# Kernel tuning notes

Hardware: AMD Instinct MI355X
Metric: run time of the kernel (lower is better)

## Reference

```python
import jax, jax.numpy as jnp
import numpy as np

N_NODES = 100000
N_EDGES = 800000
D_DATA = 100
H_DIM = 256
N_CLS = 47
K = 10
ALPHA = 0.1


def setup_inputs() -> dict:
    key = jax.random.key(0)
    ks = jax.random.split(key, 7)
    x = jax.random.normal(ks[0], (N_NODES, D_DATA), dtype=jnp.float32)
    src = jax.random.randint(ks[1], (N_EDGES,), 0, N_NODES, dtype=jnp.int32)
    dst = jax.random.randint(ks[2], (N_EDGES,), 0, N_NODES, dtype=jnp.int32)
    W1 = jax.random.normal(ks[3], (D_DATA, H_DIM), dtype=jnp.float32) / np.sqrt(D_DATA)
    b1 = jax.random.normal(ks[4], (H_DIM,), dtype=jnp.float32) * 0.01
    W2 = jax.random.normal(ks[5], (H_DIM, N_CLS), dtype=jnp.float32) / np.sqrt(H_DIM)
    b2 = jax.random.normal(ks[6], (N_CLS,), dtype=jnp.float32) * 0.01
    return {"x": x, "src": src, "dst": dst, "W1": W1, "b1": b1, "W2": W2, "b2": b2}


def reference(x, src, dst, W1, b1, W2, b2):
    # --- APPNPConv: K steps of symmetric-normalized SpMM + teleport ---
    # DGL normalizes with in-degree^{-1/2} on both message source and output.
    deg = jax.ops.segment_sum(jnp.ones((N_EDGES,), x.dtype), dst, num_segments=N_NODES)
    norm = jax.lax.rsqrt(jnp.maximum(deg, 1.0))[:, None]  # [N,1]
    h = x
    for _ in range(K):
        msg = (h * norm)[src]                              # gather src feats, [E,D]
        agg = jax.ops.segment_sum(msg, dst, num_segments=N_NODES)
        h = (1.0 - ALPHA) * (agg * norm) + ALPHA * x
    # --- feat_trans MLP (dropout inactive in eval) ---
    z = jax.nn.relu(h @ W1 + b1)
    logits = z @ W2 + b2
    return logits
```

## Files before the change

kernel.cpp:

```cpp
#include <hip/hip_runtime.h>
#include <hip/hip_fp16.h>


#define N_NODES 100000
#define N_PAD   100032
#define N_EDGES 800000
#define D_DATA  100
#define H_DIM   256
#define N_CLS   47
#define K_STEPS 10
#define ALPHA   0.1f
#define HS      128
#define MB      64

#define SCAN_NB    200
#define SCAN_CHUNK 500
#define EW_CAP (N_EDGES + 3 * N_NODES)

typedef _Float16 half8_t __attribute__((ext_vector_type(8)));
typedef float floatx4 __attribute__((ext_vector_type(4)));


__global__ void deg_kernel(const int* __restrict__ dst, int* __restrict__ deg, int e) {
    int i = blockIdx.x * blockDim.x + threadIdx.x;
    if (i < e) atomicAdd(&deg[dst[i]], 1);
}

__global__ __launch_bounds__(256) void scan_partial_kernel(
        const int* __restrict__ deg, int* __restrict__ partials) {
    __shared__ int red[256];
    int t = threadIdx.x;
    int base = blockIdx.x * SCAN_CHUNK;
    int s = 0;
    int i0 = 2 * t, i1 = 2 * t + 1;
    if (i0 < SCAN_CHUNK) s += (deg[base + i0] + 3) & ~3;
    if (i1 < SCAN_CHUNK) s += (deg[base + i1] + 3) & ~3;
    red[t] = s;
    __syncthreads();
    for (int off = 128; off > 0; off >>= 1) {
        if (t < off) red[t] += red[t + off];
        __syncthreads();
    }
    if (t == 0) partials[blockIdx.x] = red[0];
}

__global__ __launch_bounds__(256) void scan_top_kernel(
        const int* __restrict__ partials, int* __restrict__ pofs,
        int* __restrict__ row_ptr) {
    __shared__ int s[256];
    int t = threadIdx.x;
    s[t] = (t < SCAN_NB) ? partials[t] : 0;
    __syncthreads();
    for (int off = 1; off < 256; off <<= 1) {
        int v = (t >= off) ? s[t - off] : 0;
        __syncthreads();
        s[t] += v;
        __syncthreads();
    }
    if (t < SCAN_NB) pofs[t] = s[t] - partials[t];
    if (t == SCAN_NB - 1) row_ptr[N_NODES] = s[t];
}

__global__ __launch_bounds__(256) void scan_emit_kernel(
        const int* __restrict__ deg, const int* __restrict__ pofs,
        int* __restrict__ row_ptr, float* __restrict__ norm) {
    __shared__ int s[256];
    int t = threadIdx.x;
    int base = blockIdx.x * SCAN_CHUNK;
    int i0 = 2 * t, i1 = 2 * t + 1;
    int d0 = (i0 < SCAN_CHUNK) ? deg[base + i0] : 0;
    int d1 = (i1 < SCAN_CHUNK) ? deg[base + i1] : 0;
    int p0 = (d0 + 3) & ~3, p1 = (d1 + 3) & ~3;
    s[t] = p0 + p1;
    __syncthreads();
    for (int off = 1; off < 256; off <<= 1) {
        int v = (t >= off) ? s[t - off] : 0;
        __syncthreads();
        s[t] += v;
        __syncthreads();
    }
    int p = s[t] - (p0 + p1) + pofs[blockIdx.x];
    if (i0 < SCAN_CHUNK) {
        row_ptr[base + i0] = p;
        norm[base + i0] = rsqrtf((float)max(d0, 1));
    }
    if (i1 < SCAN_CHUNK) {
        row_ptr[base + i1] = p + p0;
        norm[base + i1] = rsqrtf((float)max(d1, 1));
    }
}

__global__ void scatter_kernel(const int* __restrict__ src, const int* __restrict__ dst,
                               const int* __restrict__ row_ptr, int* __restrict__ fill,
                               int* __restrict__ es, int e) {
    int i = blockIdx.x * blockDim.x + threadIdx.x;
    if (i < e) {
        int d = dst[i];
        int pos = row_ptr[d] + atomicAdd(&fill[d], 1);
        es[pos] = src[i];
    }
}

__global__ void pad_kernel(const int* __restrict__ deg, const int* __restrict__ row_ptr,
                           int* __restrict__ es, int n) {
    int i = blockIdx.x * blockDim.x + threadIdx.x;
    if (i < n) {
        int b = row_ptr[i] + deg[i];
        int e = row_ptr[i + 1];
        for (int s = b; s < e; ++s) es[s] = N_NODES;
    }
}

__global__ void pack_w1_kernel(const float* __restrict__ W1, __half* __restrict__ W1p) {
    int idx = blockIdx.x * blockDim.x + threadIdx.x;
    if (idx >= 16 * 4 * 64 * 8) return;
    int j = idx & 7;
    int lane = (idx >> 3) & 63;
    int ks = (idx >> 9) & 3;
    int nt = idx >> 11;
    int k = ks * 32 + (lane >> 4) * 8 + j;
    int n = nt * 16 + (lane & 15);
    float v = (k < D_DATA) ? W1[(size_t)k * H_DIM + n] : 0.f;
    W1p[idx] = __float2half(v);
}

__global__ void pack_w2_kernel(const float* __restrict__ W2, __half* __restrict__ W2p) {
    int idx = blockIdx.x * blockDim.x + threadIdx.x;
    if (idx >= 3 * 8 * 64 * 8) return;
    int j = idx & 7;
    int lane = (idx >> 3) & 63;
    int ks = (idx >> 9) & 7;
    int nt = idx >> 12;
    int k = ks * 32 + (lane >> 4) * 8 + j;
    int n = nt * 16 + (lane & 15);
    float v = (n < N_CLS) ? W2[(size_t)k * N_CLS + n] : 0.f;
    W2p[idx] = __float2half(v);
}

__global__ void convert_xhat_kernel(const float* __restrict__ x,
                                    const float* __restrict__ norm,
                                    __half2* __restrict__ xh, int n_half2) {
    int i = blockIdx.x * blockDim.x + threadIdx.x;
    if (i < n_half2) {
        int node = i >> 6;
        int c2 = i & 63;
        float2 v = make_float2(0.f, 0.f);
        if (node < N_NODES && c2 < D_DATA / 2) {
            float nn = norm[node];
            const float2* r = (const float2*)(x + (size_t)node * D_DATA);
            float2 xv = r[c2];
            v = make_float2(nn * xv.x, nn * xv.y);
        }
        xh[i] = __float22half2_rn(v);
    }
}

__global__ void zero_rows_kernel(__half2* __restrict__ a, __half2* __restrict__ b) {
    int i = threadIdx.x;
    if (i < 64) a[(size_t)N_NODES * (HS / 2) + i] = __half2();
    else        b[(size_t)N_NODES * (HS / 2) + (i - 64)] = __half2();
}


__global__ __launch_bounds__(256) void prop_mid_kernel(
        const __half* __restrict__ hin, const __half* __restrict__ xhat,
        const float* __restrict__ norm, const int* __restrict__ row_ptr,
        const int* __restrict__ es, __half* __restrict__ hout, int n_nodes) {
    int lane = threadIdx.x & 63;
    int node = __builtin_amdgcn_readfirstlane(blockIdx.x * 4 + (threadIdx.x >> 6));
    if (node >= n_nodes) return;
    int beg = __builtin_amdgcn_readfirstlane(row_ptr[node]);
    int end = __builtin_amdgcn_readfirstlane(row_ptr[node + 1]);
    float nn = norm[node];
    float c = (1.0f - ALPHA) * nn * nn;
    float ax = 0.f, ay = 0.f, bx = 0.f, by = 0.f;
    float cx = 0.f, cy = 0.f, dx = 0.f, dy = 0.f;
    int e = beg;
    for (; e + 8 <= end; e += 8) {
        int s[8];
#pragma unroll
        for (int j = 0; j < 8; ++j) s[j] = es[e + j];
        __half2 hv[8];
#pragma unroll
        for (int j = 0; j < 8; ++j)
            hv[j] = ((const __half2*)(hin + (size_t)s[j] * HS))[lane];
        float2 v[8];
#pragma unroll
        for (int j = 0; j < 8; ++j) v[j] = __half22float2(hv[j]);
        ax += v[0].x; ay += v[0].y;  bx += v[1].x; by += v[1].y;
        cx += v[2].x; cy += v[2].y;  dx += v[3].x; dy += v[3].y;
        ax += v[4].x; ay += v[4].y;  bx += v[5].x; by += v[5].y;
        cx += v[6].x; cy += v[6].y;  dx += v[7].x; dy += v[7].y;
    }
    if (e < end) {
        int s[4];
#pragma unroll
        for (int j = 0; j < 4; ++j) s[j] = es[e + j];
        __half2 hv[4];
#pragma unroll
        for (int j = 0; j < 4; ++j)
            hv[j] = ((const __half2*)(hin + (size_t)s[j] * HS))[lane];
#pragma unroll
        for (int j = 0; j < 4; ++j) {
            float2 v = __half22float2(hv[j]);
            ax += v.x; ay += v.y;
        }
    }
    float sx = (ax + bx) + (cx + dx);
    float sy = (ay + by) + (cy + dy);
    float2 t = __half22float2(((const __half2*)(xhat + (size_t)node * HS))[lane]);
    float2 o = make_float2(c * sx + ALPHA * t.x, c * sy + ALPHA * t.y);
    ((__half2*)(hout + (size_t)node * HS))[lane] = __float22half2_rn(o);
}

__global__ __launch_bounds__(256) void prop_final_kernel(
        const __half* __restrict__ hin, const float* __restrict__ x,
        const float* __restrict__ norm, const int* __restrict__ row_ptr,
        const int* __restrict__ es, __half* __restrict__ hout, int n_nodes) {
    int lane = threadIdx.x & 63;
    int node = __builtin_amdgcn_readfirstlane(blockIdx.x * 4 + (threadIdx.x >> 6));
    if (node >= n_nodes) return;
    int beg = __builtin_amdgcn_readfirstlane(row_ptr[node]);
    int end = __builtin_amdgcn_readfirstlane(row_ptr[node + 1]);
    float nn = norm[node];
    float c = (1.0f - ALPHA) * nn;
    float ax = 0.f, ay = 0.f, bx = 0.f, by = 0.f;
    float cx = 0.f, cy = 0.f, dx = 0.f, dy = 0.f;
    int e = beg;
    for (; e + 8 <= end; e += 8) {
        int s[8];
#pragma unroll
        for (int j = 0; j < 8; ++j) s[j] = es[e + j];
        __half2 hv[8];
#pragma unroll
        for (int j = 0; j < 8; ++j)
            hv[j] = ((const __half2*)(hin + (size_t)s[j] * HS))[lane];
        float2 v[8];
#pragma unroll
        for (int j = 0; j < 8; ++j) v[j] = __half22float2(hv[j]);
        ax += v[0].x; ay += v[0].y;  bx += v[1].x; by += v[1].y;
        cx += v[2].x; cy += v[2].y;  dx += v[3].x; dy += v[3].y;
        ax += v[4].x; ay += v[4].y;  bx += v[5].x; by += v[5].y;
        cx += v[6].x; cy += v[6].y;  dx += v[7].x; dy += v[7].y;
    }
    if (e < end) {
        int s[4];
#pragma unroll
        for (int j = 0; j < 4; ++j) s[j] = es[e + j];
        __half2 hv[4];
#pragma unroll
        for (int j = 0; j < 4; ++j)
            hv[j] = ((const __half2*)(hin + (size_t)s[j] * HS))[lane];
#pragma unroll
        for (int j = 0; j < 4; ++j) {
            float2 v = __half22float2(hv[j]);
            ax += v.x; ay += v.y;
        }
    }
    float sx = (ax + bx) + (cx + dx);
    float sy = (ay + by) + (cy + dy);
    float2 xv = make_float2(0.f, 0.f);
    if (lane < D_DATA / 2)
        xv = ((const float2*)(x + (size_t)node * D_DATA))[lane];
    float2 o = make_float2(c * sx + ALPHA * xv.x, c * sy + ALPHA * xv.y);
    ((__half2*)(hout + (size_t)node * HS))[lane] = __float22half2_rn(o);
}


#define ZP 264

__global__ __launch_bounds__(256, 4) void mlp_mfma_kernel(
        const __half* __restrict__ h16,
        const __half* __restrict__ W1p, const float* __restrict__ b1,
        const __half* __restrict__ W2p, const float* __restrict__ b2,
        float* __restrict__ out, int n_nodes) {
    __shared__ _Float16 zs[MB][ZP];
    int tid = threadIdx.x;
    int lane = tid & 63;
    int w = tid >> 6;
    int q = lane >> 4;
    int r = lane & 15;
    int node0 = blockIdx.x * MB + w * 16;

    half8_t a1[4];
#pragma unroll
    for (int ks = 0; ks < 4; ++ks)
        a1[ks] = *(const half8_t*)(h16 + (size_t)(node0 + r) * HS + ks * 32 + q * 8);

    const half8_t* w1f = (const half8_t*)W1p;
#pragma unroll 4
    for (int nt = 0; nt < 16; ++nt) {
        floatx4 acc = {0.f, 0.f, 0.f, 0.f};
#pragma unroll
        for (int ks = 0; ks < 4; ++ks) {
            half8_t b = w1f[(nt * 4 + ks) * 64 + lane];
            acc = __builtin_amdgcn_mfma_f32_16x16x32_f16(a1[ks], b, acc, 0, 0, 0);
        }
        float bb = b1[nt * 16 + r];
#pragma unroll
        for (int reg = 0; reg < 4; ++reg) {
            float zv = fmaxf(acc[reg] + bb, 0.f);
            zs[w * 16 + q * 4 + reg][nt * 16 + r] = (_Float16)zv;
        }
    }

    half8_t a2[8];
#pragma unroll
    for (int ks = 0; ks < 8; ++ks)
        a2[ks] = *(const half8_t*)&zs[w * 16 + r][ks * 32 + q * 8];

    const half8_t* w2f = (const half8_t*)W2p;
#pragma unroll
    for (int nt = 0; nt < 3; ++nt) {
        floatx4 acc = {0.f, 0.f, 0.f, 0.f};
#pragma unroll
        for (int ks = 0; ks < 8; ++ks) {
            half8_t b = w2f[(nt * 8 + ks) * 64 + lane];
            acc = __builtin_amdgcn_mfma_f32_16x16x32_f16(a2[ks], b, acc, 0, 0, 0);
        }
        int c = nt * 16 + r;
        if (c < N_CLS) {
            float bb = b2[c];
#pragma unroll
            for (int reg = 0; reg < 4; ++reg) {
                int node = node0 + q * 4 + reg;
                if (node < n_nodes)
                    out[(size_t)node * N_CLS + c] = acc[reg] + bb;
            }
        }
    }
}


static inline size_t align_up(size_t v, size_t a) { return (v + a - 1) & ~(a - 1); }

extern "C" void kernel_launch(void* const* d_in, const int* in_sizes, int n_in,
                              void* d_out, int out_size, void* d_ws, size_t ws_size,
                              hipStream_t stream) {
    const float* x   = (const float*)d_in[0];
    const int*   src = (const int*)d_in[1];
    const int*   dst = (const int*)d_in[2];
    const float* W1  = (const float*)d_in[3];
    const float* b1  = (const float*)d_in[4];
    const float* W2  = (const float*)d_in[5];
    const float* b2  = (const float*)d_in[6];
    float* out = (float*)d_out;

    char* p = (char*)d_ws;
    size_t off = 0;
    int* deg = (int*)(p + off);           off = align_up(off + N_NODES * 4, 256);
    int* row_ptr = (int*)(p + off);       off = align_up(off + (N_NODES + 1) * 4, 256);
    int* fill = (int*)(p + off);          off = align_up(off + N_NODES * 4, 256);
    float* norm = (float*)(p + off);      off = align_up(off + N_NODES * 4, 256);
    int* partials = (int*)(p + off);      off = align_up(off + SCAN_NB * 4, 256);
    int* pofs = (int*)(p + off);          off = align_up(off + SCAN_NB * 4, 256);
    __half* W1p = (__half*)(p + off);     off = align_up(off + 16 * 4 * 64 * 8 * 2, 256);
    __half* W2p = (__half*)(p + off);     off = align_up(off + 3 * 8 * 64 * 8 * 2, 256);
    int* es = (int*)(p + off);            off = align_up(off + (size_t)EW_CAP * 4, 256);
    __half* xhat = (__half*)(p + off);    off = align_up(off + (size_t)N_PAD * HS * 2, 256);
    __half* h16A = (__half*)(p + off);    off = align_up(off + (size_t)N_PAD * HS * 2, 256);
    __half* h16B = (__half*)(p + off);    off = align_up(off + (size_t)N_PAD * HS * 2, 256);
    (void)ws_size;

    hipMemsetAsync(deg, 0, N_NODES * 4, stream);
    hipMemsetAsync(fill, 0, N_NODES * 4, stream);

    int eb = (N_EDGES + 255) / 256;
    deg_kernel<<<eb, 256, 0, stream>>>(dst, deg, N_EDGES);
    scan_partial_kernel<<<SCAN_NB, 256, 0, stream>>>(deg, partials);
    scan_top_kernel<<<1, 256, 0, stream>>>(partials, pofs, row_ptr);
    scan_emit_kernel<<<SCAN_NB, 256, 0, stream>>>(deg, pofs, row_ptr, norm);
    scatter_kernel<<<eb, 256, 0, stream>>>(src, dst, row_ptr, fill, es, N_EDGES);
    pad_kernel<<<(N_NODES + 255) / 256, 256, 0, stream>>>(deg, row_ptr, es, N_NODES);
    pack_w1_kernel<<<128, 256, 0, stream>>>(W1, W1p);
    pack_w2_kernel<<<48, 256, 0, stream>>>(W2, W2p);

    int nh2 = (N_NODES + 1) * (HS / 2);
    convert_xhat_kernel<<<(nh2 + 255) / 256, 256, 0, stream>>>(x, norm, (__half2*)xhat, nh2);
    zero_rows_kernel<<<1, 128, 0, stream>>>((__half2*)h16A, (__half2*)h16B);

    int pb = N_NODES / 4;
    prop_mid_kernel<<<pb, 256, 0, stream>>>(xhat, xhat, norm, row_ptr, es, h16A, N_NODES);
    const __half* hin = h16A;
    for (int k = 1; k < K_STEPS - 1; ++k) {
        __half* ho = (k & 1) ? h16B : h16A;
        prop_mid_kernel<<<pb, 256, 0, stream>>>(hin, xhat, norm, row_ptr, es, ho, N_NODES);
        hin = ho;
    }
    prop_final_kernel<<<pb, 256, 0, stream>>>(hin, x, norm, row_ptr, es, h16B, N_NODES);

    int mb = (N_NODES + MB - 1) / MB;
    mlp_mfma_kernel<<<mb, 256, 0, stream>>>(h16B, W1p, b1, W2p, b2, out, N_NODES);
}
```

Before: 613.0 us.

## Process two nodes per wave in propagation and reuse degree-atomic slots for CSR scatter

Each propagation wave now handles two adjacent nodes, interleaving their 4-edge gather batches so more independent row loads are in flight per wave. The grid is halved to match. The degree kernel also records each edge's atomic slot, so the scatter pass needs no second atomic and no fill buffer or memset. This costs an extra 3.2MB slot array and some divergence when the two nodes have unequal degrees.

```diff
diff --git a/kernel.cpp b/kernel.cpp
--- a/kernel.cpp
+++ b/kernel.cpp
@@ -21,9 +21,10 @@
 typedef float floatx4 __attribute__((ext_vector_type(4)));
 
 
-__global__ void deg_kernel(const int* __restrict__ dst, int* __restrict__ deg, int e) {
+__global__ void deg_kernel(const int* __restrict__ dst, int* __restrict__ deg,
+                           int* __restrict__ slot, int e) {
     int i = blockIdx.x * blockDim.x + threadIdx.x;
-    if (i < e) atomicAdd(&deg[dst[i]], 1);
+    if (i < e) slot[i] = atomicAdd(&deg[dst[i]], 1);
 }
 
 __global__ __launch_bounds__(256) void scan_partial_kernel(
@@ -91,14 +92,11 @@
 }
 
 __global__ void scatter_kernel(const int* __restrict__ src, const int* __restrict__ dst,
-                               const int* __restrict__ row_ptr, int* __restrict__ fill,
+                               const int* __restrict__ slot,
+                               const int* __restrict__ row_ptr,
                                int* __restrict__ es, int e) {
     int i = blockIdx.x * blockDim.x + threadIdx.x;
-    if (i < e) {
-        int d = dst[i];
-        int pos = row_ptr[d] + atomicAdd(&fill[d], 1);
-        es[pos] = src[i];
-    }
+    if (i < e) es[row_ptr[dst[i]] + slot[i]] = src[i];
 }
 
 __global__ void pad_kernel(const int* __restrict__ deg, const int* __restrict__ row_ptr,
@@ -167,50 +165,72 @@
         const float* __restrict__ norm, const int* __restrict__ row_ptr,
         const int* __restrict__ es, __half* __restrict__ hout, int n_nodes) {
     int lane = threadIdx.x & 63;
-    int node = __builtin_amdgcn_readfirstlane(blockIdx.x * 4 + (threadIdx.x >> 6));
-    if (node >= n_nodes) return;
-    int beg = __builtin_amdgcn_readfirstlane(row_ptr[node]);
-    int end = __builtin_amdgcn_readfirstlane(row_ptr[node + 1]);
-    float nn = norm[node];
-    float c = (1.0f - ALPHA) * nn * nn;
-    float ax = 0.f, ay = 0.f, bx = 0.f, by = 0.f;
-    float cx = 0.f, cy = 0.f, dx = 0.f, dy = 0.f;
-    int e = beg;
-    for (; e + 8 <= end; e += 8) {
-        int s[8];
-#pragma unroll
-        for (int j = 0; j < 8; ++j) s[j] = es[e + j];
-        __half2 hv[8];
-#pragma unroll
-        for (int j = 0; j < 8; ++j)
-            hv[j] = ((const __half2*)(hin + (size_t)s[j] * HS))[lane];
-        float2 v[8];
-#pragma unroll
-        for (int j = 0; j < 8; ++j) v[j] = __half22float2(hv[j]);
-        ax += v[0].x; ay += v[0].y;  bx += v[1].x; by += v[1].y;
-        cx += v[2].x; cy += v[2].y;  dx += v[3].x; dy += v[3].y;
-        ax += v[4].x; ay += v[4].y;  bx += v[5].x; by += v[5].y;
-        cx += v[6].x; cy += v[6].y;  dx += v[7].x; dy += v[7].y;
-    }
-    if (e < end) {
-        int s[4];
-#pragma unroll
-        for (int j = 0; j < 4; ++j) s[j] = es[e + j];
-        __half2 hv[4];
-#pragma unroll
-        for (int j = 0; j < 4; ++j)
-            hv[j] = ((const __half2*)(hin + (size_t)s[j] * HS))[lane];
-#pragma unroll
-        for (int j = 0; j < 4; ++j) {
-            float2 v = __half22float2(hv[j]);
-            ax += v.x; ay += v.y;
-        }
-    }
-    float sx = (ax + bx) + (cx + dx);
-    float sy = (ay + by) + (cy + dy);
-    float2 t = __half22float2(((const __half2*)(xhat + (size_t)node * HS))[lane]);
-    float2 o = make_float2(c * sx + ALPHA * t.x, c * sy + ALPHA * t.y);
-    ((__half2*)(hout + (size_t)node * HS))[lane] = __float22half2_rn(o);
+    int wave = blockIdx.x * 4 + (threadIdx.x >> 6);
+    int nA = __builtin_amdgcn_readfirstlane(wave * 2);
+    if (nA >= n_nodes) return;
+    int nB = nA + 1;
+    int begA = __builtin_amdgcn_readfirstlane(row_ptr[nA]);
+    int begB = __builtin_amdgcn_readfirstlane(row_ptr[nB]);
+    int endB = __builtin_amdgcn_readfirstlane(row_ptr[nB + 1]);
+    int nbA = (begB - begA) >> 2;
+    int nbB = (endB - begB) >> 2;
+    int mb = nbA > nbB ? nbA : nbB;
+
+    float a0x = 0.f, a0y = 0.f, a1x = 0.f, a1y = 0.f;
+    float b0x = 0.f, b0y = 0.f, b1x = 0.f, b1y = 0.f;
+    for (int it = 0; it < mb; ++it) {
+        bool doA = it < nbA, doB = it < nbB;
+        int sA[4], sB[4];
+        if (doA) {
+            int e = begA + it * 4;
+#pragma unroll
+            for (int j = 0; j < 4; ++j) sA[j] = es[e + j];
+        }
+        if (doB) {
+            int e = begB + it * 4;
+#pragma unroll
+            for (int j = 0; j < 4; ++j) sB[j] = es[e + j];
+        }
+        __half2 hvA[4], hvB[4];
+        if (doA) {
+#pragma unroll
+            for (int j = 0; j < 4; ++j)
+                hvA[j] = ((const __half2*)(hin + (size_t)sA[j] * HS))[lane];
+        }
+        if (doB) {
+#pragma unroll
+            for (int j = 0; j < 4; ++j)
+                hvB[j] = ((const __half2*)(hin + (size_t)sB[j] * HS))[lane];
+        }
+        if (doA) {
+            float2 v0 = __half22float2(hvA[0]), v1 = __half22float2(hvA[1]);
+            float2 v2 = __half22float2(hvA[2]), v3 = __half22float2(hvA[3]);
+            a0x += v0.x + v2.x; a0y += v0.y + v2.y;
+            a1x += v1.x + v3.x; a1y += v1.y + v3.y;
+        }
+        if (doB) {
+            float2 v0 = __half22float2(hvB[0]), v1 = __half22float2(hvB[1]);
+            float2 v2 = __half22float2(hvB[2]), v3 = __half22float2(hvB[3]);
+            b0x += v0.x + v2.x; b0y += v0.y + v2.y;
+            b1x += v1.x + v3.x; b1y += v1.y + v3.y;
+        }
+    }
+    {
+        float nn = norm[nA];
+        float c = (1.0f - ALPHA) * nn * nn;
+        float2 t = __half22float2(((const __half2*)(xhat + (size_t)nA * HS))[lane]);
+        float2 o = make_float2(c * (a0x + a1x) + ALPHA * t.x,
+                               c * (a0y + a1y) + ALPHA * t.y);
+        ((__half2*)(hout + (size_t)nA * HS))[lane] = __float22half2_rn(o);
+    }
+    {
+        float nn = norm[nB];
+        float c = (1.0f - ALPHA) * nn * nn;
+        float2 t = __half22float2(((const __half2*)(xhat + (size_t)nB * HS))[lane]);
+        float2 o = make_float2(c * (b0x + b1x) + ALPHA * t.x,
+                               c * (b0y + b1y) + ALPHA * t.y);
+        ((__half2*)(hout + (size_t)nB * HS))[lane] = __float22half2_rn(o);
+    }
 }
 
 __global__ __launch_bounds__(256) void prop_final_kernel(
@@ -218,52 +238,74 @@
         const float* __restrict__ norm, const int* __restrict__ row_ptr,
         const int* __restrict__ es, __half* __restrict__ hout, int n_nodes) {
     int lane = threadIdx.x & 63;
-    int node = __builtin_amdgcn_readfirstlane(blockIdx.x * 4 + (threadIdx.x >> 6));
-    if (node >= n_nodes) return;
-    int beg = __builtin_amdgcn_readfirstlane(row_ptr[node]);
-    int end = __builtin_amdgcn_readfirstlane(row_ptr[node + 1]);
-    float nn = norm[node];
-    float c = (1.0f - ALPHA) * nn;
-    float ax = 0.f, ay = 0.f, bx = 0.f, by = 0.f;
-    float cx = 0.f, cy = 0.f, dx = 0.f, dy = 0.f;
-    int e = beg;
-    for (; e + 8 <= end; e += 8) {
-        int s[8];
-#pragma unroll
-        for (int j = 0; j < 8; ++j) s[j] = es[e + j];
-        __half2 hv[8];
-#pragma unroll
-        for (int j = 0; j < 8; ++j)
-            hv[j] = ((const __half2*)(hin + (size_t)s[j] * HS))[lane];
-        float2 v[8];
-#pragma unroll
-        for (int j = 0; j < 8; ++j) v[j] = __half22float2(hv[j]);
-        ax += v[0].x; ay += v[0].y;  bx += v[1].x; by += v[1].y;
-        cx += v[2].x; cy += v[2].y;  dx += v[3].x; dy += v[3].y;
-        ax += v[4].x; ay += v[4].y;  bx += v[5].x; by += v[5].y;
-        cx += v[6].x; cy += v[6].y;  dx += v[7].x; dy += v[7].y;
-    }
-    if (e < end) {
-        int s[4];
-#pragma unroll
-        for (int j = 0; j < 4; ++j) s[j] = es[e + j];
-        __half2 hv[4];
-#pragma unroll
-        for (int j = 0; j < 4; ++j)
-            hv[j] = ((const __half2*)(hin + (size_t)s[j] * HS))[lane];
-#pragma unroll
-        for (int j = 0; j < 4; ++j) {
-            float2 v = __half22float2(hv[j]);
-            ax += v.x; ay += v.y;
-        }
-    }
-    float sx = (ax + bx) + (cx + dx);
-    float sy = (ay + by) + (cy + dy);
-    float2 xv = make_float2(0.f, 0.f);
-    if (lane < D_DATA / 2)
-        xv = ((const float2*)(x + (size_t)node * D_DATA))[lane];
-    float2 o = make_float2(c * sx + ALPHA * xv.x, c * sy + ALPHA * xv.y);
-    ((__half2*)(hout + (size_t)node * HS))[lane] = __float22half2_rn(o);
+    int wave = blockIdx.x * 4 + (threadIdx.x >> 6);
+    int nA = __builtin_amdgcn_readfirstlane(wave * 2);
+    if (nA >= n_nodes) return;
+    int nB = nA + 1;
+    int begA = __builtin_amdgcn_readfirstlane(row_ptr[nA]);
+    int begB = __builtin_amdgcn_readfirstlane(row_ptr[nB]);
+    int endB = __builtin_amdgcn_readfirstlane(row_ptr[nB + 1]);
+    int nbA = (begB - begA) >> 2;
+    int nbB = (endB - begB) >> 2;
+    int mb = nbA > nbB ? nbA : nbB;
+
+    float a0x = 0.f, a0y = 0.f, a1x = 0.f, a1y = 0.f;
+    float b0x = 0.f, b0y = 0.f, b1x = 0.f, b1y = 0.f;
+    for (int it = 0; it < mb; ++it) {
+        bool doA = it < nbA, doB = it < nbB;
+        int sA[4], sB[4];
+        if (doA) {
+            int e = begA + it * 4;
+#pragma unroll
+            for (int j = 0; j < 4; ++j) sA[j] = es[e + j];
+        }
+        if (doB) {
+            int e = begB + it * 4;
+#pragma unroll
+            for (int j = 0; j < 4; ++j) sB[j] = es[e + j];
+        }
+        __half2 hvA[4], hvB[4];
+        if (doA) {
+#pragma unroll
+            for (int j = 0; j < 4; ++j)
+                hvA[j] = ((const __half2*)(hin + (size_t)sA[j] * HS))[lane];
+        }
+        if (doB) {
+#pragma unroll
+            for (int j = 0; j < 4; ++j)
+                hvB[j] = ((const __half2*)(hin + (size_t)sB[j] * HS))[lane];
+        }
+        if (doA) {
+            float2 v0 = __half22float2(hvA[0]), v1 = __half22float2(hvA[1]);
+            float2 v2 = __half22float2(hvA[2]), v3 = __half22float2(hvA[3]);
+            a0x += v0.x + v2.x; a0y += v0.y + v2.y;
+            a1x += v1.x + v3.x; a1y += v1.y + v3.y;
+        }
+        if (doB) {
+            float2 v0 = __half22float2(hvB[0]), v1 = __half22float2(hvB[1]);
+            float2 v2 = __half22float2(hvB[2]), v3 = __half22float2(hvB[3]);
+            b0x += v0.x + v2.x; b0y += v0.y + v2.y;
+            b1x += v1.x + v3.x; b1y += v1.y + v3.y;
+        }
+    }
+    {
+        float c = (1.0f - ALPHA) * norm[nA];
+        float2 xv = make_float2(0.f, 0.f);
+        if (lane < D_DATA / 2)
+            xv = ((const float2*)(x + (size_t)nA * D_DATA))[lane];
+        float2 o = make_float2(c * (a0x + a1x) + ALPHA * xv.x,
+                               c * (a0y + a1y) + ALPHA * xv.y);
+        ((__half2*)(hout + (size_t)nA * HS))[lane] = __float22half2_rn(o);
+    }
+    {
+        float c = (1.0f - ALPHA) * norm[nB];
+        float2 xv = make_float2(0.f, 0.f);
+        if (lane < D_DATA / 2)
+            xv = ((const float2*)(x + (size_t)nB * D_DATA))[lane];
+        float2 o = make_float2(c * (b0x + b1x) + ALPHA * xv.x,
+                               c * (b0y + b1y) + ALPHA * xv.y);
+        ((__half2*)(hout + (size_t)nB * HS))[lane] = __float22half2_rn(o);
+    }
 }
 
 
@@ -350,7 +392,7 @@
     size_t off = 0;
     int* deg = (int*)(p + off);           off = align_up(off + N_NODES * 4, 256);
     int* row_ptr = (int*)(p + off);       off = align_up(off + (N_NODES + 1) * 4, 256);
-    int* fill = (int*)(p + off);          off = align_up(off + N_NODES * 4, 256);
+    int* slot = (int*)(p + off);          off = align_up(off + (size_t)N_EDGES * 4, 256);
     float* norm = (float*)(p + off);      off = align_up(off + N_NODES * 4, 256);
     int* partials = (int*)(p + off);      off = align_up(off + SCAN_NB * 4, 256);
     int* pofs = (int*)(p + off);          off = align_up(off + SCAN_NB * 4, 256);
@@ -363,14 +405,13 @@
     (void)ws_size;
 
     hipMemsetAsync(deg, 0, N_NODES * 4, stream);
-    hipMemsetAsync(fill, 0, N_NODES * 4, stream);
 
     int eb = (N_EDGES + 255) / 256;
-    deg_kernel<<<eb, 256, 0, stream>>>(dst, deg, N_EDGES);
+    deg_kernel<<<eb, 256, 0, stream>>>(dst, deg, slot, N_EDGES);
     scan_partial_kernel<<<SCAN_NB, 256, 0, stream>>>(deg, partials);
     scan_top_kernel<<<1, 256, 0, stream>>>(partials, pofs, row_ptr);
     scan_emit_kernel<<<SCAN_NB, 256, 0, stream>>>(deg, pofs, row_ptr, norm);
-    scatter_kernel<<<eb, 256, 0, stream>>>(src, dst, row_ptr, fill, es, N_EDGES);
+    scatter_kernel<<<eb, 256, 0, stream>>>(src, dst, slot, row_ptr, es, N_EDGES);
     pad_kernel<<<(N_NODES + 255) / 256, 256, 0, stream>>>(deg, row_ptr, es, N_NODES);
     pack_w1_kernel<<<128, 256, 0, stream>>>(W1, W1p);
     pack_w2_kernel<<<48, 256, 0, stream>>>(W2, W2p);
@@ -379,7 +420,7 @@
     convert_xhat_kernel<<<(nh2 + 255) / 256, 256, 0, stream>>>(x, norm, (__half2*)xhat, nh2);
     zero_rows_kernel<<<1, 128, 0, stream>>>((__half2*)h16A, (__half2*)h16B);
 
-    int pb = N_NODES / 4;
+    int pb = (N_NODES / 2) / 4;
     prop_mid_kernel<<<pb, 256, 0, stream>>>(xhat, xhat, norm, row_ptr, es, h16A, N_NODES);
     const __half* hin = h16A;
     for (int k = 1; k < K_STEPS - 1; ++k) {
```

After: 554.8 us, median of 2. 9.5% less time.
